# Kernel optimization log

Measured on AMD Instinct MI355X. Metric: run time of the kernel, lower is better.

Reference implementation:

```python
import jax, jax.numpy as jnp
import numpy as np

B = 8192          # batch_size (pairs of embeddings)
D = 1024          # embedding dim
C = 1024          # number of classes (torch.unique(labels) -> 0..C-1, all present)
EPS = 1e-12       # F.normalize eps


def _normalize(x):
    # F.normalize(x, dim=1): x / max(||x||_2, eps)
    n = jnp.linalg.norm(x, axis=1, keepdims=True)
    return x / jnp.maximum(n, EPS)


def setup_inputs() -> dict:
    key = jax.random.key(0)
    k1, k2, k3 = jax.random.split(key, 3)
    emb_i = jax.random.normal(k1, (B, D), dtype=jnp.float32)
    emb_j = jax.random.normal(k2, (B, D), dtype=jnp.float32)
    # shuffled arange % C guarantees every class id in [0, C) appears,
    # matching torch.unique(labels) == arange(C)
    labels = jax.random.permutation(k3, jnp.arange(B, dtype=jnp.int32) % C).astype(jnp.int64)
    return {"emb_i": emb_i, "emb_j": emb_j, "labels": labels}


def reference(emb_i, emb_j, labels):
    z_i = _normalize(emb_i)  # [B, D]
    z_j = _normalize(emb_j)  # [B, D]

    # vectorized replacement of the per-label python loop:
    # class_prototypes[c] = mean of z_i rows with label c  (segment mean)
    seg_sum = jax.ops.segment_sum(z_i, labels, num_segments=C)                    # [C, D]
    seg_cnt = jax.ops.segment_sum(jnp.ones((B,), z_i.dtype), labels, num_segments=C)  # [C]
    prototypes = seg_sum / seg_cnt[:, None]                                       # [C, D]

    # similarity = 2 - cdist(z_j, prototypes, p=2)
    d2 = (jnp.sum(z_j * z_j, axis=1)[:, None]
          + jnp.sum(prototypes * prototypes, axis=1)[None, :]
          - 2.0 * z_j @ prototypes.T)                                             # [B, C]
    sim = 2.0 - jnp.sqrt(jnp.maximum(d2, 0.0))

    # match_matrix: labels_proto (arange(C)) == labels[:, None]
    match = (jnp.arange(C)[None, :] == labels[:, None]).astype(sim.dtype)         # [B, C]

    # BCEWithLogitsLoss (mean reduction), numerically stable via log_sigmoid
    loss = jnp.mean(-(match * jax.nn.log_sigmoid(sim)
                      + (1.0 - match) * jax.nn.log_sigmoid(-sim)))
    return loss
```

## Files before the change

kernel.cpp:

```cpp
#include <hip/hip_runtime.h>

#define B_N 8192
#define D_N 1024
#define C_N 1024
#define BM 256
#define BN 128
#define BK 64

typedef __attribute__((ext_vector_type(8))) __bf16 bf16x8;
typedef __attribute__((ext_vector_type(16))) float floatx16;

__device__ inline unsigned short f2bf(float f) {
  union { float f; unsigned int u; } cv; cv.f = f;
  unsigned int b = cv.u;
  unsigned int r = (b + 0x7FFFu + ((b >> 16) & 1u)) >> 16;
  return (unsigned short)r;
}
__device__ inline float d4(const float4 a) {
  return a.x * a.x + a.y * a.y + a.z * a.z + a.w * a.w;
}
__device__ inline ushort4 pk4(const float4 v, const float s) {
  ushort4 u;
  u.x = f2bf(v.x * s); u.y = f2bf(v.y * s);
  u.z = f2bf(v.z * s); u.w = f2bf(v.w * s);
  return u;
}

__global__ __launch_bounds__(256) void prep_kernel(
    const float* __restrict__ emb_i, const float* __restrict__ emb_j,
    const int* __restrict__ labels,
    unsigned short* __restrict__ z_j, unsigned short* __restrict__ proto,
    float* __restrict__ p2, float* __restrict__ out) {
  __shared__ float sx[4][8];
  __shared__ int list[8];
  __shared__ int scnt;

  const int t = threadIdx.x;
  const int lane = t & 63;
  const int wid = t >> 6;
  const int blk = blockIdx.x;

  if (t == 0) scnt = 0;
  if (blk == 0 && t == 0) out[0] = 0.0f;

#pragma unroll
  for (int it = 0; it < 2; ++it) {
    const int row = blk * 8 + it * 4 + wid;
    const float4* src = (const float4*)(emb_j + (size_t)row * D_N);
    const float4 v0 = src[lane], v1 = src[lane + 64];
    const float4 v2 = src[lane + 128], v3 = src[lane + 192];
    float ss = d4(v0) + d4(v1) + d4(v2) + d4(v3);
    for (int o = 32; o; o >>= 1) ss += __shfl_xor(ss, o, 64);
    const float inv = 1.0f / fmaxf(sqrtf(ss), 1e-12f);
    ushort4* dst = (ushort4*)(z_j + (size_t)row * D_N);
    dst[lane] = pk4(v0, inv);
    dst[lane + 64] = pk4(v1, inv);
    dst[lane + 128] = pk4(v2, inv);
    dst[lane + 192] = pk4(v3, inv);
  }

  const int c = blk;
  __syncthreads();
  const int4* lab4 = (const int4*)labels;
  for (int i = 0; i < 8; ++i) {
    const int q = i * 256 + t;
    const int4 L = lab4[q];
    const int base = q * 4;
    if (L.x == c) list[atomicAdd(&scnt, 1) & 7] = base;
    if (L.y == c) list[atomicAdd(&scnt, 1) & 7] = base + 1;
    if (L.z == c) list[atomicAdd(&scnt, 1) & 7] = base + 2;
    if (L.w == c) list[atomicAdd(&scnt, 1) & 7] = base + 3;
  }
  __syncthreads();

  const float* base = emb_i + wid * 256;
  float4 v[8];
  float ss[8];
#pragma unroll
  for (int k = 0; k < 8; ++k) {
    v[k] = ((const float4*)(base + (size_t)list[k] * D_N))[lane];
    ss[k] = d4(v[k]);
  }
#pragma unroll
  for (int k = 0; k < 8; ++k)
    for (int o = 32; o; o >>= 1) ss[k] += __shfl_xor(ss[k], o, 64);
  if (lane == 0) {
#pragma unroll
    for (int k = 0; k < 8; ++k) sx[wid][k] = ss[k];
  }
  __syncthreads();

  float4 a = make_float4(0.f, 0.f, 0.f, 0.f);
#pragma unroll
  for (int k = 0; k < 8; ++k) {
    const float tot = sx[0][k] + sx[1][k] + sx[2][k] + sx[3][k];
    const float iv = 1.0f / fmaxf(sqrtf(tot), 1e-12f);
    a.x += v[k].x * iv; a.y += v[k].y * iv;
    a.z += v[k].z * iv; a.w += v[k].w * iv;
  }
  a.x *= 0.125f; a.y *= 0.125f; a.z *= 0.125f; a.w *= 0.125f;

  float pp = d4(a);
  for (int o = 32; o; o >>= 1) pp += __shfl_xor(pp, o, 64);
  __syncthreads();
  if (lane == 0) sx[wid][0] = pp;
  __syncthreads();
  if (t == 0) p2[c] = sx[0][0] + sx[1][0] + sx[2][0] + sx[3][0];

  ((ushort4*)(proto + (size_t)c * D_N + wid * 256))[lane] = pk4(a, 1.0f);
}

#define GLOAD(gp, lp)                                                        \
  __builtin_amdgcn_global_load_lds(                                          \
      (const __attribute__((address_space(1))) void*)(gp),                   \
      (__attribute__((address_space(3))) void*)(lp), 16, 0, 0)

__global__ __launch_bounds__(512) void gemm_loss_kernel(
    const unsigned short* __restrict__ Zj,
    const unsigned short* __restrict__ P,
    const float* __restrict__ p2,
    const int* __restrict__ labels,
    float* __restrict__ out) {
  __shared__ __align__(16) unsigned short lds[3 * 24576];
  __shared__ float sred[8];

  const int t = threadIdx.x;
  const int lane = t & 63;
  const int wid = t >> 6;
  const int wm = (wid >> 1) * 64;
  const int wn = (wid & 1) * 64;
  const int bm = blockIdx.x;
  const int bn = blockIdx.y;

  floatx16 acc[2][2];
#pragma unroll
  for (int i = 0; i < 2; ++i)
#pragma unroll
    for (int j = 0; j < 2; ++j)
      for (int r = 0; r < 16; ++r) acc[i][j][r] = 0.f;

  const int srow = t >> 3;
  const int g = (t & 7) ^ (srow & 7);
  const unsigned short* Ag = Zj + (size_t)(bm * BM + srow) * D_N + g * 8;
  const unsigned short* Bg = P + (size_t)(bn * BN + srow) * D_N + g * 8;
  unsigned short* const Al0 = (unsigned short*)lds + t * 8;
  unsigned short* const Bl0 = (unsigned short*)lds + 16384 + t * 8;

  const int ar0 = (wm + (lane & 31)) * BK;
  const int ar1 = ar0 + 32 * BK;
  const int br0 = 16384 + (wn + (lane & 31)) * BK;
  const int br1 = br0 + 32 * BK;
  const int h = lane >> 5;
  const int q = lane & 7;

#define STAGE(bi, kt)                                                        \
  {                                                                          \
    const int _bo = (bi) * 24576;                                            \
    const int _k0 = (kt) * BK;                                               \
    GLOAD(Ag + (size_t)0 * 64 * D_N + _k0, Al0 + _bo + 0 * 4096);            \
    GLOAD(Ag + (size_t)1 * 64 * D_N + _k0, Al0 + _bo + 1 * 4096);            \
    GLOAD(Ag + (size_t)2 * 64 * D_N + _k0, Al0 + _bo + 2 * 4096);            \
    GLOAD(Ag + (size_t)3 * 64 * D_N + _k0, Al0 + _bo + 3 * 4096);            \
    GLOAD(Bg + (size_t)0 * 64 * D_N + _k0, Bl0 + _bo + 0 * 4096);            \
    GLOAD(Bg + (size_t)1 * 64 * D_N + _k0, Bl0 + _bo + 1 * 4096);            \
  }

#define COMPUTE(bi)                                                          \
  {                                                                          \
    const unsigned short* Lb = (const unsigned short*)lds + (bi) * 24576;    \
    _Pragma("unroll") for (int kk = 0; kk < 4; ++kk) {                       \
      const int swz = ((kk * 2 + h) ^ q) << 3;                               \
      bf16x8 a0 = *(const bf16x8*)(Lb + ar0 + swz);                          \
      bf16x8 a1 = *(const bf16x8*)(Lb + ar1 + swz);                          \
      bf16x8 b0 = *(const bf16x8*)(Lb + br0 + swz);                          \
      bf16x8 b1 = *(const bf16x8*)(Lb + br1 + swz);                          \
      acc[0][0] = __builtin_amdgcn_mfma_f32_32x32x16_bf16(a0, b0, acc[0][0], 0, 0, 0); \
      acc[0][1] = __builtin_amdgcn_mfma_f32_32x32x16_bf16(a0, b1, acc[0][1], 0, 0, 0); \
      acc[1][0] = __builtin_amdgcn_mfma_f32_32x32x16_bf16(a1, b0, acc[1][0], 0, 0, 0); \
      acc[1][1] = __builtin_amdgcn_mfma_f32_32x32x16_bf16(a1, b1, acc[1][1], 0, 0, 0); \
    }                                                                        \
  }

  STAGE(0, 0);
  STAGE(1, 1);

  int cur = 0;
  for (int kt = 0; kt < 14; ++kt) {
    const int nb = (cur + 2 >= 3) ? (cur - 1) : (cur + 2);
    STAGE(nb, kt + 2);
    asm volatile("s_waitcnt vmcnt(12)" ::: "memory");
    __builtin_amdgcn_s_barrier();
    __builtin_amdgcn_sched_barrier(0);
    __builtin_amdgcn_s_setprio(1);
    COMPUTE(cur);
    __builtin_amdgcn_s_setprio(0);
    __builtin_amdgcn_sched_barrier(0);
    __builtin_amdgcn_s_barrier();
    cur = (cur == 2) ? 0 : cur + 1;
  }
  asm volatile("s_waitcnt vmcnt(6)" ::: "memory");
  __builtin_amdgcn_s_barrier();
  __builtin_amdgcn_sched_barrier(0);
  COMPUTE(cur);
  cur = (cur == 2) ? 0 : cur + 1;
  asm volatile("s_waitcnt vmcnt(0)" ::: "memory");
  __builtin_amdgcn_s_barrier();
  __builtin_amdgcn_sched_barrier(0);
  COMPUTE(cur);

  const int colbase = bn * BN + wn + (lane & 31);
  float lsum = 0.f;
#pragma unroll
  for (int mb = 0; mb < 2; ++mb) {
    const int rowbase = bm * BM + wm + mb * 32 + 4 * h;
    int labv[16];
#pragma unroll
    for (int reg = 0; reg < 16; ++reg)
      labv[reg] = labels[rowbase + (reg & 3) + 8 * (reg >> 2)];
#pragma unroll
    for (int nb2 = 0; nb2 < 2; ++nb2) {
      const int col = colbase + nb2 * 32;
      const float p2c = p2[col];
#pragma unroll
      for (int reg = 0; reg < 16; ++reg) {
        const float dot = acc[mb][nb2][reg];
        const float d2 = 1.0f + p2c - 2.0f * dot;
        const float s = 2.0f - sqrtf(fmaxf(d2, 0.0f));
        const float sp = fmaxf(s, 0.0f) + log1pf(expf(-fabsf(s)));
        lsum += sp - ((labv[reg] == col) ? s : 0.0f);
      }
    }
  }
  for (int o = 32; o; o >>= 1) lsum += __shfl_xor(lsum, o, 64);
  if (lane == 0) sred[wid] = lsum;
  __syncthreads();
  if (t == 0) {
    float bs = 0.f;
#pragma unroll
    for (int w = 0; w < 8; ++w) bs += sred[w];
    atomicAdd(out, bs * (1.0f / ((float)B_N * (float)C_N)));
  }
}

extern "C" void kernel_launch(void* const* d_in, const int* in_sizes, int n_in,
                              void* d_out, int out_size, void* d_ws, size_t ws_size,
                              hipStream_t stream) {
  const float* emb_i = (const float*)d_in[0];
  const float* emb_j = (const float*)d_in[1];
  const int* labels = (const int*)d_in[2];
  float* out = (float*)d_out;

  char* ws = (char*)d_ws;
  unsigned short* z_j = (unsigned short*)ws;
  unsigned short* proto = (unsigned short*)(ws + (size_t)16777216);
  float* p2 = (float*)(ws + (size_t)18874368);

  prep_kernel<<<dim3(C_N), 256, 0, stream>>>(emb_i, emb_j, labels, z_j,
                                             proto, p2, out);
  gemm_loss_kernel<<<dim3(B_N / BM, C_N / BN), 512, 0, stream>>>(z_j, proto,
                                                                 p2, labels, out);
}
```

Before: 149.9 us.

## Split GEMM k-tile into two phases interleaving global loads with MFMA

Restructures the main GEMM loop so each 64-wide k-tile is computed in two half phases. Each phase reads its LDS fragments up front, then issues half of the next stage's global-to-LDS loads before running its MFMAs. The intent is to spread global load issue across the compute and let it overlap with the MFMA work. The wait before each tile is tightened to vmcnt(6) to match the new issue order. In exchange it adds an extra workgroup barrier and an lgkmcnt(0) wait per phase, and holds more fragment registers live at once.

```diff
diff --git a/kernel.cpp b/kernel.cpp
--- a/kernel.cpp
+++ b/kernel.cpp
@@ -153,60 +153,75 @@
   const int h = lane >> 5;
   const int q = lane & 7;
 
-#define STAGE(bi, kt)                                                        \
-  {                                                                          \
-    const int _bo = (bi) * 24576;                                            \
-    const int _k0 = (kt) * BK;                                               \
-    GLOAD(Ag + (size_t)0 * 64 * D_N + _k0, Al0 + _bo + 0 * 4096);            \
-    GLOAD(Ag + (size_t)1 * 64 * D_N + _k0, Al0 + _bo + 1 * 4096);            \
-    GLOAD(Ag + (size_t)2 * 64 * D_N + _k0, Al0 + _bo + 2 * 4096);            \
-    GLOAD(Ag + (size_t)3 * 64 * D_N + _k0, Al0 + _bo + 3 * 4096);            \
-    GLOAD(Bg + (size_t)0 * 64 * D_N + _k0, Bl0 + _bo + 0 * 4096);            \
-    GLOAD(Bg + (size_t)1 * 64 * D_N + _k0, Bl0 + _bo + 1 * 4096);            \
-  }
-
-#define COMPUTE(bi)                                                          \
+#define STAGE_A(bi, k2)                                                      \
+  do {                                                                       \
+    unsigned short* _al = Al0 + (bi) * 24576;                                \
+    GLOAD(Ag + (size_t)0 * 64 * D_N + (k2), _al + 0 * 4096);                 \
+    GLOAD(Ag + (size_t)1 * 64 * D_N + (k2), _al + 1 * 4096);                 \
+    GLOAD(Ag + (size_t)2 * 64 * D_N + (k2), _al + 2 * 4096);                 \
+  } while (0)
+#define STAGE_B(bi, k2)                                                      \
+  do {                                                                       \
+    unsigned short* _al = Al0 + (bi) * 24576;                                \
+    unsigned short* _bl = Bl0 + (bi) * 24576;                                \
+    GLOAD(Ag + (size_t)3 * 64 * D_N + (k2), _al + 3 * 4096);                 \
+    GLOAD(Bg + (size_t)0 * 64 * D_N + (k2), _bl + 0 * 4096);                 \
+    GLOAD(Bg + (size_t)1 * 64 * D_N + (k2), _bl + 1 * 4096);                 \
+  } while (0)
+#define NOGL ((void)0)
+
+#define PHASE(bi, kkb, GL)                                                   \
   {                                                                          \
     const unsigned short* Lb = (const unsigned short*)lds + (bi) * 24576;    \
-    _Pragma("unroll") for (int kk = 0; kk < 4; ++kk) {                       \
-      const int swz = ((kk * 2 + h) ^ q) << 3;                               \
-      bf16x8 a0 = *(const bf16x8*)(Lb + ar0 + swz);                          \
-      bf16x8 a1 = *(const bf16x8*)(Lb + ar1 + swz);                          \
-      bf16x8 b0 = *(const bf16x8*)(Lb + br0 + swz);                          \
-      bf16x8 b1 = *(const bf16x8*)(Lb + br1 + swz);                          \
-      acc[0][0] = __builtin_amdgcn_mfma_f32_32x32x16_bf16(a0, b0, acc[0][0], 0, 0, 0); \
-      acc[0][1] = __builtin_amdgcn_mfma_f32_32x32x16_bf16(a0, b1, acc[0][1], 0, 0, 0); \
-      acc[1][0] = __builtin_amdgcn_mfma_f32_32x32x16_bf16(a1, b0, acc[1][0], 0, 0, 0); \
-      acc[1][1] = __builtin_amdgcn_mfma_f32_32x32x16_bf16(a1, b1, acc[1][1], 0, 0, 0); \
-    }                                                                        \
-  }
-
-  STAGE(0, 0);
-  STAGE(1, 1);
+    const int s0 = ((((kkb) + 0) * 2 + h) ^ q) << 3;                         \
+    const int s1 = ((((kkb) + 1) * 2 + h) ^ q) << 3;                         \
+    bf16x8 a0k0 = *(const bf16x8*)(Lb + ar0 + s0);                           \
+    bf16x8 a1k0 = *(const bf16x8*)(Lb + ar1 + s0);                           \
+    bf16x8 b0k0 = *(const bf16x8*)(Lb + br0 + s0);                           \
+    bf16x8 b1k0 = *(const bf16x8*)(Lb + br1 + s0);                           \
+    bf16x8 a0k1 = *(const bf16x8*)(Lb + ar0 + s1);                           \
+    bf16x8 a1k1 = *(const bf16x8*)(Lb + ar1 + s1);                           \
+    bf16x8 b0k1 = *(const bf16x8*)(Lb + br0 + s1);                           \
+    bf16x8 b1k1 = *(const bf16x8*)(Lb + br1 + s1);                           \
+    GL;                                                                      \
+    asm volatile("s_waitcnt lgkmcnt(0)" ::: "memory");                       \
+    __builtin_amdgcn_sched_barrier(0);                                       \
+    __builtin_amdgcn_s_setprio(1);                                           \
+    acc[0][0] = __builtin_amdgcn_mfma_f32_32x32x16_bf16(a0k0, b0k0, acc[0][0], 0, 0, 0); \
+    acc[0][1] = __builtin_amdgcn_mfma_f32_32x32x16_bf16(a0k0, b1k0, acc[0][1], 0, 0, 0); \
+    acc[1][0] = __builtin_amdgcn_mfma_f32_32x32x16_bf16(a1k0, b0k0, acc[1][0], 0, 0, 0); \
+    acc[1][1] = __builtin_amdgcn_mfma_f32_32x32x16_bf16(a1k0, b1k0, acc[1][1], 0, 0, 0); \
+    acc[0][0] = __builtin_amdgcn_mfma_f32_32x32x16_bf16(a0k1, b0k1, acc[0][0], 0, 0, 0); \
+    acc[0][1] = __builtin_amdgcn_mfma_f32_32x32x16_bf16(a0k1, b1k1, acc[0][1], 0, 0, 0); \
+    acc[1][0] = __builtin_amdgcn_mfma_f32_32x32x16_bf16(a1k1, b0k1, acc[1][0], 0, 0, 0); \
+    acc[1][1] = __builtin_amdgcn_mfma_f32_32x32x16_bf16(a1k1, b1k1, acc[1][1], 0, 0, 0); \
+    __builtin_amdgcn_s_setprio(0);                                           \
+    __builtin_amdgcn_sched_barrier(0);                                       \
+    __builtin_amdgcn_s_barrier();                                            \
+  }
+
+  STAGE_A(0, 0); STAGE_B(0, 0);
+  STAGE_A(1, BK); STAGE_B(1, BK);
 
   int cur = 0;
   for (int kt = 0; kt < 14; ++kt) {
-    const int nb = (cur + 2 >= 3) ? (cur - 1) : (cur + 2);
-    STAGE(nb, kt + 2);
-    asm volatile("s_waitcnt vmcnt(12)" ::: "memory");
+    const int nb = (cur == 0) ? 2 : cur - 1;
+    const int k2 = (kt + 2) * BK;
+    asm volatile("s_waitcnt vmcnt(6)" ::: "memory");
     __builtin_amdgcn_s_barrier();
-    __builtin_amdgcn_sched_barrier(0);
-    __builtin_amdgcn_s_setprio(1);
-    COMPUTE(cur);
-    __builtin_amdgcn_s_setprio(0);
-    __builtin_amdgcn_sched_barrier(0);
-    __builtin_amdgcn_s_barrier();
+    PHASE(cur, 0, STAGE_A(nb, k2));
+    PHASE(cur, 2, STAGE_B(nb, k2));
     cur = (cur == 2) ? 0 : cur + 1;
   }
   asm volatile("s_waitcnt vmcnt(6)" ::: "memory");
   __builtin_amdgcn_s_barrier();
-  __builtin_amdgcn_sched_barrier(0);
-  COMPUTE(cur);
+  PHASE(cur, 0, NOGL);
+  PHASE(cur, 2, NOGL);
   cur = (cur == 2) ? 0 : cur + 1;
   asm volatile("s_waitcnt vmcnt(0)" ::: "memory");
   __builtin_amdgcn_s_barrier();
-  __builtin_amdgcn_sched_barrier(0);
-  COMPUTE(cur);
+  PHASE(cur, 0, NOGL);
+  PHASE(cur, 2, NOGL);
 
   const int colbase = bn * BN + wn + (lane & 31);
   float lsum = 0.f;
```

Result: faster. 146.1 us (-2.5%).
